# Optimization experiments

Hardware: AMD Instinct MI355X
Metric: run time of the kernel (lower is better)

The kernel has to match this reference:

```python
import jax, jax.numpy as jnp
import numpy as np

TAU = 0.1
LAM = 1.0
LOG_NOISE = 1e-12
COS_EPS = 1e-8      # torch CosineSimilarity eps
NORM_EPS = 1e-12    # torch F.normalize eps


def setup_inputs() -> dict:
    key = jax.random.key(0)
    k1, k2, k3, k4 = jax.random.split(key, 4)
    B, D, S = 8192, 128, 64
    z1s = jax.random.normal(k1, (B, D), dtype=jnp.float32)
    z2s = jax.random.normal(k2, (B, D), dtype=jnp.float32)
    z1_c_outs = jax.random.uniform(k3, (B, S), dtype=jnp.float32)
    z1_subject_labels = jax.random.normal(k4, (B, S), dtype=jnp.float32)
    return {"z1s": z1s, "z2s": z2s, "z1_c_outs": z1_c_outs,
            "z1_subject_labels": z1_subject_labels}


def _l2_normalize(x, eps):
    # normalize rows; clamp norm from below like torch
    n = jnp.linalg.norm(x, axis=1, keepdims=True)
    return x / jnp.maximum(n, eps)


def reference(z1s, z2s, z1_c_outs, z1_subject_labels):
    B = z1s.shape[0]
    z1 = z1s.reshape(B, -1)
    z2 = z2s.reshape(B, -1)
    n1 = _l2_normalize(z1, COS_EPS)
    n2 = _l2_normalize(z2, COS_EPS)

    # all-pairs cosine similarities, scaled by temperature
    S12 = jnp.matmul(n1, n2.T) / TAU   # [B, B] sim(z1_i, z2_k)/tau
    S11 = jnp.matmul(n1, n1.T) / TAU   # [B, B] sim(z1_i, z1_k)/tau

    e12 = jnp.exp(S12)
    e11 = jnp.exp(S11)
    numerator = jnp.diagonal(e12)                       # exp(sim(z1_i, z2_i)/tau)
    # denom_i = sum_k e12[i,k] + sum_{k != i} e11[i,k]
    denom = e12.sum(axis=1) + e11.sum(axis=1) - jnp.diagonal(e11)
    contrastive = -jnp.log(LOG_NOISE + numerator / denom)
    loss = contrastive.sum() / (B * (2.0 * B - 1.0))

    # adversarial term: -lam * log(1 - normalized_pred[i, argmax(label_i)])
    c = _l2_normalize(z1_c_outs, NORM_EPS)
    j = jnp.argmax(z1_subject_labels, axis=1)           # [B] int
    picked = c[jnp.arange(B), j]
    loss = loss + LAM * (-jnp.log(LOG_NOISE + 1.0 - picked)).sum()
    return loss
```

## Files before the change

### kernel.cpp

```cpp
#include <hip/hip_runtime.h>
#include <hip/hip_bf16.h>
#include <math.h>


#define NROWS 8192
#define DFEAT 128

typedef __bf16 bf16_t;
typedef __bf16 bf16x8 __attribute__((ext_vector_type(8)));
typedef __bf16 bf16x2 __attribute__((ext_vector_type(2)));
typedef float  f32x4  __attribute__((ext_vector_type(4)));

__device__ __forceinline__ float fexp2(float x) {
#if __has_builtin(__builtin_amdgcn_exp2f)
  return __builtin_amdgcn_exp2f(x);
#else
  return exp2f(x);
#endif
}

__device__ __forceinline__ void stage16(const void* gsrc, void* ldst) {
  __builtin_amdgcn_global_load_lds(
      (const __attribute__((address_space(1))) unsigned int*)gsrc,
      (__attribute__((address_space(3))) unsigned int*)ldst, 16, 0, 0);
}

#define WAITVM(n) asm volatile("s_waitcnt vmcnt(" #n ")" ::: "memory")

__global__ __launch_bounds__(1024)
void sa_prep_kernel(const float* __restrict__ z1,
                    const float* __restrict__ z2,
                    bf16_t* __restrict__ Abuf,
                    bf16_t* __restrict__ Kc,
                    float* __restrict__ numv,
                    float* __restrict__ d11v) {
  __shared__ __align__(16) bf16_t LA[16][136];
  __shared__ __align__(16) bf16_t LK2[16][136];
  __shared__ __align__(16) bf16_t LK1[16][136];

  int wave = threadIdx.x >> 6;
  int lane = threadIdx.x & 63;
  int tile = blockIdx.x;
  int row  = tile * 16 + wave;

  float2 a = ((const float2*)(z1 + (size_t)row * DFEAT))[lane];
  float2 b = ((const float2*)(z2 + (size_t)row * DFEAT))[lane];

  float s1  = a.x * a.x + a.y * a.y;
  float s2  = b.x * b.x + b.y * b.y;
  float s12 = a.x * b.x + a.y * b.y;
#pragma unroll
  for (int m = 32; m; m >>= 1) {
    s1  += __shfl_xor(s1, m, 64);
    s2  += __shfl_xor(s2, m, 64);
    s12 += __shfl_xor(s12, m, 64);
  }
  float r1 = 1.0f / fmaxf(sqrtf(s1), 1e-8f);
  float r2 = 1.0f / fmaxf(sqrtf(s2), 1e-8f);

  const float SCL = 14.426950408889634f;

  bf16x2 av;  av[0] = (bf16_t)(a.x * r1 * SCL); av[1] = (bf16_t)(a.y * r1 * SCL);
  bf16x2 k2v; k2v[0] = (bf16_t)(b.x * r2);      k2v[1] = (bf16_t)(b.y * r2);
  bf16x2 k1v; k1v[0] = (bf16_t)(a.x * r1);      k1v[1] = (bf16_t)(a.y * r1);

  *(bf16x2*)&LA[wave][2 * lane]  = av;
  *(bf16x2*)&LK2[wave][2 * lane] = k2v;
  *(bf16x2*)&LK1[wave][2 * lane] = k1v;

  if (lane == 0) {
    numv[row] = expf(10.0f * s12 * r1 * r2);
    d11v[row] = expf(10.0f * s1 * r1 * r1);
  }
  __syncthreads();

  int t = threadIdx.x;
  if (t < 768) {
    int sel = t >> 8;
    int u   = t & 255;
    int kf  = u >> 6;
    int qk  = (u >> 4) & 3;
    int r16 = u & 15;
    const bf16_t* Ls = (sel == 0) ? &LA[0][0]
                     : (sel == 1) ? &LK2[0][0] : &LK1[0][0];
    bf16x8 v = *(const bf16x8*)(Ls + r16 * 136 + kf * 32 + qk * 8);
    bf16_t* dst = (sel == 0) ? (Abuf + (size_t)tile * 2048)
                : (sel == 1) ? (Kc + (size_t)tile * 2048)
                             : (Kc + (size_t)(512 + tile) * 2048);
    *(bf16x8*)(dst + u * 8) = v;
  }
}

__global__ __launch_bounds__(256, 4)
void sa_main_kernel(const bf16_t* __restrict__ Abuf,
                    const bf16_t* __restrict__ Kc,
                    float* __restrict__ T2) {
  __shared__ __align__(16) bf16_t bsm[4][4096];

  int wave = threadIdx.x >> 6;
  int lane = threadIdx.x & 63;
  int quad = lane >> 4;

  int id  = blockIdx.x;
  int swz = (id & 7) * 128 + (id >> 3);
  int bx  = swz & 31;
  int by  = swz >> 5;
  int rowBase = bx * 256 + wave * 64;
  int colBase = by * 512;

  const bf16x8* ap = (const bf16x8*)Abuf + (size_t)(rowBase >> 4) * 256 + lane;
  bf16x8 afrag[4][4];
#pragma unroll
  for (int s = 0; s < 4; ++s)
#pragma unroll
    for (int kfi = 0; kfi < 4; ++kfi)
      afrag[s][kfi] = ap[(s * 4 + kfi) * 64];

  f32x4 sums[4];
#pragma unroll
  for (int s = 0; s < 4; ++s) sums[s] = (f32x4){0.f, 0.f, 0.f, 0.f};

  const char* bsrc = (const char*)Kc + (size_t)(colBase >> 4) * 4096 +
                     (size_t)wave * 2048 + (size_t)lane * 16;
  char* lbase = (char*)&bsm[0][0] + (size_t)wave * 2048;

  auto stagePhase = [&](int p) {
    const char* src = bsrc + (size_t)p * 8192;
    char* dst = lbase + (size_t)(p & 3) * 8192;
    stage16(src, dst);
    stage16(src + 1024, dst + 1024);
  };

  auto computePhase = [&](int pbuf) {
    const bf16_t* base = &bsm[0][0] + pbuf * 4096;
#pragma unroll
    for (int tt = 0; tt < 2; ++tt) {
      const bf16x8* bs = (const bf16x8*)(base + tt * 2048);
      bf16x8 bfr[4];
#pragma unroll
      for (int kfi = 0; kfi < 4; ++kfi) bfr[kfi] = bs[kfi * 64 + lane];
      __builtin_amdgcn_s_setprio(1);
#pragma unroll
      for (int s = 0; s < 4; ++s) {
        f32x4 c = {0.f, 0.f, 0.f, 0.f};
#pragma unroll
        for (int kfi = 0; kfi < 4; ++kfi)
          c = __builtin_amdgcn_mfma_f32_16x16x32_bf16(afrag[s][kfi], bfr[kfi],
                                                      c, 0, 0, 0);
#pragma unroll
        for (int r = 0; r < 4; ++r) sums[s][r] += fexp2(c[r]);
      }
      __builtin_amdgcn_s_setprio(0);
    }
  };

  stagePhase(0);
  stagePhase(1);
  stagePhase(2);

#pragma unroll 1
  for (int p = 0; p < 13; ++p) {
    WAITVM(4);
    __builtin_amdgcn_s_barrier();
    __builtin_amdgcn_sched_barrier(0);
    stagePhase(p + 3);
    computePhase(p & 3);
  }
  WAITVM(4);
  __builtin_amdgcn_s_barrier();
  __builtin_amdgcn_sched_barrier(0);
  computePhase(1);
  WAITVM(2);
  __builtin_amdgcn_s_barrier();
  __builtin_amdgcn_sched_barrier(0);
  computePhase(2);
  WAITVM(0);
  __builtin_amdgcn_s_barrier();
  __builtin_amdgcn_sched_barrier(0);
  computePhase(3);

  int l15 = lane & 15;
#pragma unroll
  for (int s = 0; s < 4; ++s) {
#pragma unroll
    for (int r = 0; r < 4; ++r) {
      float v = sums[s][r];
      v += __shfl_xor(v, 1, 64);
      v += __shfl_xor(v, 2, 64);
      v += __shfl_xor(v, 4, 64);
      v += __shfl_xor(v, 8, 64);
      if (l15 == 0)
        T2[(size_t)(rowBase + s * 16 + quad * 4 + r) * 32 + by] = v;
    }
  }
}

__global__ __launch_bounds__(256)
void sa_final_adv_kernel(const float* __restrict__ T2,
                         const float* __restrict__ numv,
                         const float* __restrict__ d11v,
                         const float* __restrict__ c,
                         const float* __restrict__ lab,
                         float* __restrict__ partial) {
  int wave = threadIdx.x >> 6;
  int lane = threadIdx.x & 63;
  int row  = blockIdx.x * 4 + wave;

  float cv = c[row * 64 + lane];
  float lv = lab[row * 64 + lane];
  float tv = (lane < 32) ? T2[(size_t)row * 32 + lane] : 0.0f;

  float ss = cv * cv;
  float bestv = lv;
  int   besti = lane;
#pragma unroll
  for (int m = 32; m; m >>= 1) {
    ss += __shfl_xor(ss, m, 64);
    tv += __shfl_xor(tv, m, 64);
    float ov = __shfl_xor(bestv, m, 64);
    int   oi = __shfl_xor(besti, m, 64);
    if (ov > bestv || (ov == bestv && oi < besti)) { bestv = ov; besti = oi; }
  }
  float picked = __shfl(cv, besti, 64) / fmaxf(sqrtf(ss), 1e-12f);

  float term = 0.0f;
  if (lane == 0) {
    float denom = tv - d11v[row];
    term = -logf(1e-12f + numv[row] / denom) * (1.0f / 134209536.0f)
           - logf(1e-12f + 1.0f - picked);
  }

  __shared__ float wacc[4];
  if (lane == 0) wacc[wave] = term;
  __syncthreads();
  if (threadIdx.x == 0)
    partial[blockIdx.x] = wacc[0] + wacc[1] + wacc[2] + wacc[3];
}

__global__ __launch_bounds__(256)
void sa_reduce_kernel(const float* __restrict__ partial,
                      float* __restrict__ out) {
  float v = 0.0f;
#pragma unroll
  for (int i = 0; i < 8; ++i) v += partial[threadIdx.x + 256 * i];
#pragma unroll
  for (int m = 32; m; m >>= 1) v += __shfl_xor(v, m, 64);
  __shared__ float wacc[4];
  if ((threadIdx.x & 63) == 0) wacc[threadIdx.x >> 6] = v;
  __syncthreads();
  if (threadIdx.x == 0) out[0] = wacc[0] + wacc[1] + wacc[2] + wacc[3];
}

extern "C" void kernel_launch(void* const* d_in, const int* in_sizes, int n_in,
                              void* d_out, int out_size, void* d_ws,
                              size_t ws_size, hipStream_t stream) {
  const float* z1  = (const float*)d_in[0];
  const float* z2  = (const float*)d_in[1];
  const float* co  = (const float*)d_in[2];
  const float* lab = (const float*)d_in[3];
  float* out = (float*)d_out;

  char* ws = (char*)d_ws;
  bf16_t* Abuf  = (bf16_t*)ws;
  bf16_t* Kc    = (bf16_t*)(ws + 2u * 1024 * 1024);
  float*  T2    = (float*)(ws + 6u * 1024 * 1024);
  float*  numv  = (float*)(ws + 7u * 1024 * 1024);
  float*  d11v  = numv + NROWS;
  float*  part  = d11v + NROWS;

  sa_prep_kernel<<<NROWS / 16, 1024, 0, stream>>>(z1, z2, Abuf, Kc, numv,
                                                  d11v);
  sa_main_kernel<<<1024, 256, 0, stream>>>(Abuf, Kc, T2);
  sa_final_adv_kernel<<<NROWS / 4, 256, 0, stream>>>(T2, numv, d11v, co, lab,
                                                     part);
  sa_reduce_kernel<<<1, 256, 0, stream>>>(part, out);
}
```

Baseline: 129.2 us.

## Use 512-thread main blocks with triple buffering and atomic final reduction

The main similarity kernel now runs 512-thread blocks covering 512 rows each, so every staged column tile feeds eight waves instead of four. Staging uses three LDS buffers with one barrier per phase, and blocks are remapped so each XCD handles a contiguous column range. The MFMA priority bump is narrowed to the MFMA chain only. The separate reduce kernel is replaced by atomicAdd into the output, which is zeroed in the prep kernel. This saves one launch and halves the column-tile traffic, at the cost of a nondeterministic float summation order and fewer blocks in flight.

```diff
diff --git a/kernel.cpp b/kernel.cpp
--- a/kernel.cpp
+++ b/kernel.cpp
@@ -33,7 +33,8 @@
                     bf16_t* __restrict__ Abuf,
                     bf16_t* __restrict__ Kc,
                     float* __restrict__ numv,
-                    float* __restrict__ d11v) {
+                    float* __restrict__ d11v,
+                    float* __restrict__ out) {
   __shared__ __align__(16) bf16_t LA[16][136];
   __shared__ __align__(16) bf16_t LK2[16][136];
   __shared__ __align__(16) bf16_t LK1[16][136];
@@ -71,6 +72,7 @@
   if (lane == 0) {
     numv[row] = expf(10.0f * s12 * r1 * r2);
     d11v[row] = expf(10.0f * s1 * r1 * r1);
+    if (row == 0) out[0] = 0.0f;
   }
   __syncthreads();
 
@@ -91,21 +93,22 @@
   }
 }
 
-__global__ __launch_bounds__(256, 4)
+__global__ __launch_bounds__(512, 4)
 void sa_main_kernel(const bf16_t* __restrict__ Abuf,
                     const bf16_t* __restrict__ Kc,
                     float* __restrict__ T2) {
-  __shared__ __align__(16) bf16_t bsm[4][4096];
+  __shared__ __align__(16) bf16_t bsm[3][4096];
 
   int wave = threadIdx.x >> 6;
   int lane = threadIdx.x & 63;
   int quad = lane >> 4;
 
-  int id  = blockIdx.x;
-  int swz = (id & 7) * 128 + (id >> 3);
-  int bx  = swz & 31;
-  int by  = swz >> 5;
-  int rowBase = bx * 256 + wave * 64;
+  int id     = blockIdx.x;
+  int xcd    = id & 7;
+  int within = id >> 3;
+  int by     = xcd * 4 + (within >> 4);
+  int bx     = within & 15;
+  int rowBase = bx * 512 + wave * 64;
   int colBase = by * 512;
 
   const bf16x8* ap = (const bf16x8*)Abuf + (size_t)(rowBase >> 4) * 256 + lane;
@@ -121,63 +124,55 @@
   for (int s = 0; s < 4; ++s) sums[s] = (f32x4){0.f, 0.f, 0.f, 0.f};
 
   const char* bsrc = (const char*)Kc + (size_t)(colBase >> 4) * 4096 +
-                     (size_t)wave * 2048 + (size_t)lane * 16;
-  char* lbase = (char*)&bsm[0][0] + (size_t)wave * 2048;
+                     (size_t)wave * 1024 + (size_t)lane * 16;
+  char* lw = (char*)&bsm[0][0] + (size_t)wave * 1024;
 
   auto stagePhase = [&](int p) {
-    const char* src = bsrc + (size_t)p * 8192;
-    char* dst = lbase + (size_t)(p & 3) * 8192;
-    stage16(src, dst);
-    stage16(src + 1024, dst + 1024);
+    stage16(bsrc + (size_t)p * 8192, lw + (size_t)(p % 3) * 8192);
   };
 
-  auto computePhase = [&](int pbuf) {
-    const bf16_t* base = &bsm[0][0] + pbuf * 4096;
+  auto computePhase = [&](int p) {
+    const bf16_t* base = &bsm[0][0] + (p % 3) * 4096;
 #pragma unroll
     for (int tt = 0; tt < 2; ++tt) {
       const bf16x8* bs = (const bf16x8*)(base + tt * 2048);
       bf16x8 bfr[4];
 #pragma unroll
       for (int kfi = 0; kfi < 4; ++kfi) bfr[kfi] = bs[kfi * 64 + lane];
-      __builtin_amdgcn_s_setprio(1);
 #pragma unroll
       for (int s = 0; s < 4; ++s) {
         f32x4 c = {0.f, 0.f, 0.f, 0.f};
+        __builtin_amdgcn_s_setprio(1);
 #pragma unroll
         for (int kfi = 0; kfi < 4; ++kfi)
           c = __builtin_amdgcn_mfma_f32_16x16x32_bf16(afrag[s][kfi], bfr[kfi],
                                                       c, 0, 0, 0);
+        __builtin_amdgcn_s_setprio(0);
 #pragma unroll
         for (int r = 0; r < 4; ++r) sums[s][r] += fexp2(c[r]);
       }
-      __builtin_amdgcn_s_setprio(0);
     }
   };
 
   stagePhase(0);
   stagePhase(1);
-  stagePhase(2);
+  WAITVM(1);
+  __builtin_amdgcn_s_barrier();
+  __builtin_amdgcn_sched_barrier(0);
 
 #pragma unroll 1
-  for (int p = 0; p < 13; ++p) {
-    WAITVM(4);
+  for (int p = 0; p < 14; ++p) {
+    stagePhase(p + 2);
+    computePhase(p);
+    WAITVM(1);
     __builtin_amdgcn_s_barrier();
     __builtin_amdgcn_sched_barrier(0);
-    stagePhase(p + 3);
-    computePhase(p & 3);
-  }
-  WAITVM(4);
-  __builtin_amdgcn_s_barrier();
-  __builtin_amdgcn_sched_barrier(0);
-  computePhase(1);
-  WAITVM(2);
-  __builtin_amdgcn_s_barrier();
-  __builtin_amdgcn_sched_barrier(0);
-  computePhase(2);
+  }
+  computePhase(14);
   WAITVM(0);
   __builtin_amdgcn_s_barrier();
   __builtin_amdgcn_sched_barrier(0);
-  computePhase(3);
+  computePhase(15);
 
   int l15 = lane & 15;
 #pragma unroll
@@ -201,7 +196,7 @@
                          const float* __restrict__ d11v,
                          const float* __restrict__ c,
                          const float* __restrict__ lab,
-                         float* __restrict__ partial) {
+                         float* __restrict__ out) {
   int wave = threadIdx.x >> 6;
   int lane = threadIdx.x & 63;
   int row  = blockIdx.x * 4 + wave;
@@ -234,21 +229,7 @@
   if (lane == 0) wacc[wave] = term;
   __syncthreads();
   if (threadIdx.x == 0)
-    partial[blockIdx.x] = wacc[0] + wacc[1] + wacc[2] + wacc[3];
-}
-
-__global__ __launch_bounds__(256)
-void sa_reduce_kernel(const float* __restrict__ partial,
-                      float* __restrict__ out) {
-  float v = 0.0f;
-#pragma unroll
-  for (int i = 0; i < 8; ++i) v += partial[threadIdx.x + 256 * i];
-#pragma unroll
-  for (int m = 32; m; m >>= 1) v += __shfl_xor(v, m, 64);
-  __shared__ float wacc[4];
-  if ((threadIdx.x & 63) == 0) wacc[threadIdx.x >> 6] = v;
-  __syncthreads();
-  if (threadIdx.x == 0) out[0] = wacc[0] + wacc[1] + wacc[2] + wacc[3];
+    atomicAdd(out, wacc[0] + wacc[1] + wacc[2] + wacc[3]);
 }
 
 extern "C" void kernel_launch(void* const* d_in, const int* in_sizes, int n_in,
@@ -266,12 +247,10 @@
   float*  T2    = (float*)(ws + 6u * 1024 * 1024);
   float*  numv  = (float*)(ws + 7u * 1024 * 1024);
   float*  d11v  = numv + NROWS;
-  float*  part  = d11v + NROWS;
 
   sa_prep_kernel<<<NROWS / 16, 1024, 0, stream>>>(z1, z2, Abuf, Kc, numv,
-                                                  d11v);
-  sa_main_kernel<<<1024, 256, 0, stream>>>(Abuf, Kc, T2);
+                                                  d11v, out);
+  sa_main_kernel<<<512, 512, 0, stream>>>(Abuf, Kc, T2);
   sa_final_adv_kernel<<<NROWS / 4, 256, 0, stream>>>(T2, numv, d11v, co, lab,
-                                                     part);
-  sa_reduce_kernel<<<1, 256, 0, stream>>>(part, out);
-}
+                                                     out);
+}
```

New measurement: 130.3 us. About the same (+0.9%).

## Stage whole B column tile once in LDS and drop streamed pipeline

Applied to the files above, without the earlier changes.

The main GEMM+exp kernel now uses 512-thread blocks covering 512 rows by 256 columns. Each block loads its full 64 KB B tile into LDS once behind a single barrier, replacing the 4-stage global_load_lds ring with per-phase barriers. Waves start at staggered LDS sub-tiles, and the column-partial sums are written transposed as vector stores with 64 column blocks. This trims barrier and wait overhead and halves how often each A row is reused against loaded B. The costs are a serial load-then-compute start with no overlap, and 64 KB of LDS per block, which limits occupancy.

```diff
diff --git a/kernel.cpp b/kernel.cpp
--- a/kernel.cpp
+++ b/kernel.cpp
@@ -24,8 +24,6 @@
       (const __attribute__((address_space(1))) unsigned int*)gsrc,
       (__attribute__((address_space(3))) unsigned int*)ldst, 16, 0, 0);
 }
-
-#define WAITVM(n) asm volatile("s_waitcnt vmcnt(" #n ")" ::: "memory")
 
 __global__ __launch_bounds__(1024)
 void sa_prep_kernel(const float* __restrict__ z1,
@@ -91,22 +89,22 @@
   }
 }
 
-__global__ __launch_bounds__(256, 4)
+__global__ __launch_bounds__(512, 4)
 void sa_main_kernel(const bf16_t* __restrict__ Abuf,
                     const bf16_t* __restrict__ Kc,
-                    float* __restrict__ T2) {
-  __shared__ __align__(16) bf16_t bsm[4][4096];
+                    float* __restrict__ T2t) {
+  __shared__ __align__(16) bf16_t bsm[32768];
 
   int wave = threadIdx.x >> 6;
   int lane = threadIdx.x & 63;
   int quad = lane >> 4;
 
-  int id  = blockIdx.x;
-  int swz = (id & 7) * 128 + (id >> 3);
-  int bx  = swz & 31;
-  int by  = swz >> 5;
-  int rowBase = bx * 256 + wave * 64;
-  int colBase = by * 512;
+  int id     = blockIdx.x;
+  int xcd    = id & 7;
+  int within = id >> 3;
+  int by     = xcd * 8 + (within >> 4);
+  int bx     = within & 15;
+  int rowBase = bx * 512 + wave * 64;
 
   const bf16x8* ap = (const bf16x8*)Abuf + (size_t)(rowBase >> 4) * 256 + lane;
   bf16x8 afrag[4][4];
@@ -116,72 +114,47 @@
     for (int kfi = 0; kfi < 4; ++kfi)
       afrag[s][kfi] = ap[(s * 4 + kfi) * 64];
 
+  const char* src = (const char*)Kc + (size_t)by * 65536 +
+                    (size_t)wave * 8192 + (size_t)lane * 16;
+  char* dst = (char*)&bsm[0] + wave * 8192;
+#pragma unroll
+  for (int i = 0; i < 8; ++i) stage16(src + i * 1024, dst + i * 1024);
+
+  __syncthreads();
+
   f32x4 sums[4];
 #pragma unroll
   for (int s = 0; s < 4; ++s) sums[s] = (f32x4){0.f, 0.f, 0.f, 0.f};
 
-  const char* bsrc = (const char*)Kc + (size_t)(colBase >> 4) * 4096 +
-                     (size_t)wave * 2048 + (size_t)lane * 16;
-  char* lbase = (char*)&bsm[0][0] + (size_t)wave * 2048;
-
-  auto stagePhase = [&](int p) {
-    const char* src = bsrc + (size_t)p * 8192;
-    char* dst = lbase + (size_t)(p & 3) * 8192;
-    stage16(src, dst);
-    stage16(src + 1024, dst + 1024);
-  };
-
-  auto computePhase = [&](int pbuf) {
-    const bf16_t* base = &bsm[0][0] + pbuf * 4096;
+#pragma unroll 1
+  for (int i = 0; i < 8; ++i) {
+    int p = (wave + i) & 7;
+    const bf16_t* base = &bsm[0] + p * 4096;
 #pragma unroll
     for (int tt = 0; tt < 2; ++tt) {
       const bf16x8* bs = (const bf16x8*)(base + tt * 2048);
       bf16x8 bfr[4];
 #pragma unroll
       for (int kfi = 0; kfi < 4; ++kfi) bfr[kfi] = bs[kfi * 64 + lane];
-      __builtin_amdgcn_s_setprio(1);
 #pragma unroll
       for (int s = 0; s < 4; ++s) {
         f32x4 c = {0.f, 0.f, 0.f, 0.f};
+        __builtin_amdgcn_s_setprio(1);
 #pragma unroll
         for (int kfi = 0; kfi < 4; ++kfi)
           c = __builtin_amdgcn_mfma_f32_16x16x32_bf16(afrag[s][kfi], bfr[kfi],
                                                       c, 0, 0, 0);
+        __builtin_amdgcn_s_setprio(0);
 #pragma unroll
         for (int r = 0; r < 4; ++r) sums[s][r] += fexp2(c[r]);
       }
-      __builtin_amdgcn_s_setprio(0);
     }
-  };
-
-  stagePhase(0);
-  stagePhase(1);
-  stagePhase(2);
-
-#pragma unroll 1
-  for (int p = 0; p < 13; ++p) {
-    WAITVM(4);
-    __builtin_amdgcn_s_barrier();
-    __builtin_amdgcn_sched_barrier(0);
-    stagePhase(p + 3);
-    computePhase(p & 3);
-  }
-  WAITVM(4);
-  __builtin_amdgcn_s_barrier();
-  __builtin_amdgcn_sched_barrier(0);
-  computePhase(1);
-  WAITVM(2);
-  __builtin_amdgcn_s_barrier();
-  __builtin_amdgcn_sched_barrier(0);
-  computePhase(2);
-  WAITVM(0);
-  __builtin_amdgcn_s_barrier();
-  __builtin_amdgcn_sched_barrier(0);
-  computePhase(3);
+  }
 
   int l15 = lane & 15;
 #pragma unroll
   for (int s = 0; s < 4; ++s) {
+    f32x4 st;
 #pragma unroll
     for (int r = 0; r < 4; ++r) {
       float v = sums[s][r];
@@ -189,14 +162,15 @@
       v += __shfl_xor(v, 2, 64);
       v += __shfl_xor(v, 4, 64);
       v += __shfl_xor(v, 8, 64);
-      if (l15 == 0)
-        T2[(size_t)(rowBase + s * 16 + quad * 4 + r) * 32 + by] = v;
+      st[r] = v;
     }
+    if (l15 == 0)
+      *(f32x4*)(T2t + (size_t)by * 8192 + rowBase + s * 16 + quad * 4) = st;
   }
 }
 
 __global__ __launch_bounds__(256)
-void sa_final_adv_kernel(const float* __restrict__ T2,
+void sa_final_adv_kernel(const float* __restrict__ T2t,
                          const float* __restrict__ numv,
                          const float* __restrict__ d11v,
                          const float* __restrict__ c,
@@ -208,7 +182,7 @@
 
   float cv = c[row * 64 + lane];
   float lv = lab[row * 64 + lane];
-  float tv = (lane < 32) ? T2[(size_t)row * 32 + lane] : 0.0f;
+  float tv = T2t[(size_t)lane * 8192 + row];
 
   float ss = cv * cv;
   float bestv = lv;
@@ -263,15 +237,15 @@
   char* ws = (char*)d_ws;
   bf16_t* Abuf  = (bf16_t*)ws;
   bf16_t* Kc    = (bf16_t*)(ws + 2u * 1024 * 1024);
-  float*  T2    = (float*)(ws + 6u * 1024 * 1024);
-  float*  numv  = (float*)(ws + 7u * 1024 * 1024);
+  float*  T2t   = (float*)(ws + 6u * 1024 * 1024);
+  float*  numv  = (float*)(ws + 8u * 1024 * 1024);
   float*  d11v  = numv + NROWS;
   float*  part  = d11v + NROWS;
 
   sa_prep_kernel<<<NROWS / 16, 1024, 0, stream>>>(z1, z2, Abuf, Kc, numv,
                                                   d11v);
-  sa_main_kernel<<<1024, 256, 0, stream>>>(Abuf, Kc, T2);
-  sa_final_adv_kernel<<<NROWS / 4, 256, 0, stream>>>(T2, numv, d11v, co, lab,
+  sa_main_kernel<<<1024, 512, 0, stream>>>(Abuf, Kc, T2t);
+  sa_final_adv_kernel<<<NROWS / 4, 256, 0, stream>>>(T2t, numv, d11v, co, lab,
                                                      part);
   sa_reduce_kernel<<<1, 256, 0, stream>>>(part, out);
 }
```

Result: faster. 106.0 us (-18.0%).
